# Optimization experiments

Hardware: AMD Instinct MI355X
Metric: run time of the kernel (lower is better)

## Reference

```python
import jax, jax.numpy as jnp
import numpy as np

NUM_NEIGHBORS = (10, 25)  # FLAGS.num_neighbors = '10_25'
MAX_DEGREE = 64
L = 2  # num encoder layers


def _sample(nodes, neighbors_out, neighbors_in, key):
    """Multi-hop uniform neighbor sampling (shuffle columns + slice, as in TF code)."""
    samples = [nodes]
    support = 1
    supports = [1]
    for k in range(L):
        t = L - 1 - k
        n = NUM_NEIGHBORS[t]
        support *= 2 * n
        supports.append(support)
        key, k1, k2 = jax.random.split(key, 3)
        # tf.transpose(tf.random.shuffle(tf.transpose(x))) shuffles neighbor slots
        # with ONE permutation shared across all rows, then slices first n.
        cols_out = jax.random.permutation(k1, MAX_DEGREE)[:n]
        cols_in = jax.random.permutation(k2, MAX_DEGREE)[:n]
        nout = neighbors_out[samples[k]][:, cols_out]  # [prev, n]
        nin = neighbors_in[samples[k]][:, cols_in]     # [prev, n]
        samples.append(jnp.concatenate([nout, nin], axis=1).reshape(-1))
    return samples, supports


def _gc(self_v, nei_out, nei_in, W):
    # GraphConvolution: mean-aggregate out/in neighbors, concat with self, linear, sigmoid.
    agg = jnp.concatenate([self_v, nei_out.mean(axis=1), nei_in.mean(axis=1)], axis=-1)
    return jax.nn.sigmoid(agg @ W)


def _aggregate(inputs, supports, layer, W, B):
    h_hop = []
    for hop in range(L - layer):
        n = NUM_NEIGHBORS[L - hop - 1]
        nei = inputs[hop + 1].reshape(B * supports[hop], 2 * n, -1)
        self_v = inputs[hop].reshape(B * supports[hop], -1)
        h_hop.append(_gc(self_v, nei[:, :n], nei[:, n:], W))
    return h_hop


def _forward(nodes1, nodes2, neighbors_out, neighbors_in, features,
             W_in, W_mean, W_std, W_pi, W_ag, W_ad, Wd_mean, Wd_std, Wd_pi):
    B = nodes1.shape[0]
    key = jax.random.key(42)
    k1, k2 = jax.random.split(key)
    s1, sup1 = _sample(nodes1, neighbors_out, neighbors_in, k1)
    s2, sup2 = _sample(nodes2, neighbors_out, neighbors_in, k2)
    in1 = [features[s] for s in s1]  # hop-wise gathered features
    in2 = [features[s] for s in s2]
    # layer 0: shared input GC
    h1 = _aggregate(in1, sup1, 0, W_in, B)
    h2 = _aggregate(in2, sup2, 0, W_in, B)
    # layer 1: parameter heads (mean/std/pi/alpha)
    h_mean1 = _aggregate(h1, sup1, 1, W_mean, B)[0]
    h_mean2 = _aggregate(h2, sup2, 1, W_mean, B)[0]
    h_std1 = _aggregate(h1, sup1, 1, W_std, B)[0]
    h_std2 = _aggregate(h2, sup2, 1, W_std, B)[0]
    h_pi1 = _aggregate(h1, sup1, 1, W_pi, B)[0]
    h_pi2 = _aggregate(h2, sup2, 1, W_pi, B)[0]
    # final fully-connected projections (act = identity)
    z_mean1 = h_mean1 @ Wd_mean
    z_mean2 = h_mean2 @ Wd_mean
    z_std1 = h_std1 @ Wd_std
    z_std2 = h_std2 @ Wd_std
    pi_logit1 = h_pi1 @ Wd_pi
    pi_logit2 = h_pi2 @ Wd_pi
    return jnp.stack([z_mean1, z_std1, pi_logit1, z_mean2, z_std2, pi_logit2])


def setup_inputs() -> dict:
    key = jax.random.key(0)
    ks = jax.random.split(key, 16)
    N, F, B = 200000, 128, 256
    E, D = 128, 64
    inp = {
        'nodes1': jax.random.randint(ks[0], (B,), 0, N, dtype=jnp.int32),
        'nodes2': jax.random.randint(ks[1], (B,), 0, N, dtype=jnp.int32),
        'neighbors_out': jax.random.randint(ks[2], (N, MAX_DEGREE), 0, N, dtype=jnp.int32),
        'neighbors_in': jax.random.randint(ks[3], (N, MAX_DEGREE), 0, N, dtype=jnp.int32),
        'features': jax.random.normal(ks[4], (N, F), dtype=jnp.float32),
        'W_in': jax.random.normal(ks[5], (3 * F, E), dtype=jnp.float32) * 0.05,
        'W_mean': jax.random.normal(ks[6], (3 * E, E), dtype=jnp.float32) * 0.05,
        'W_std': jax.random.normal(ks[7], (3 * E, E), dtype=jnp.float32) * 0.05,
        'W_pi': jax.random.normal(ks[8], (3 * E, E), dtype=jnp.float32) * 0.05,
        'W_ag': jax.random.normal(ks[9], (3 * E, E), dtype=jnp.float32) * 0.05,
        'W_ad': jax.random.normal(ks[10], (3 * E, E), dtype=jnp.float32) * 0.05,
        'Wd_mean': jax.random.normal(ks[11], (E, D), dtype=jnp.float32) * 0.05,
        'Wd_std': jax.random.normal(ks[12], (E, D), dtype=jnp.float32) * 0.05,
        'Wd_pi': jax.random.normal(ks[13], (E, D), dtype=jnp.float32) * 0.05,
    }
    return inp


def reference(nodes1, nodes2, neighbors_out, neighbors_in, features,
              W_in, W_mean, W_std, W_pi, W_ag, W_ad, Wd_mean, Wd_std, Wd_pi):
    return _forward(nodes1, nodes2, neighbors_out, neighbors_in, features,
                    W_in, W_mean, W_std, W_pi, W_ag, W_ad, Wd_mean, Wd_std, Wd_pi)
```

## Files before the change

### kernel.cpp

```cpp
#include <hip/hip_runtime.h>
#include <stdint.h>
#include <math.h>

#define FDIM 128
#define KDIM 384
#define NROWS 26112

struct Cols { int o25[25]; int i25[25]; int o10[10]; int i10[10]; };
struct ColsBoth { Cols c[2]; };

static inline uint32_t rotl32(uint32_t x, uint32_t r){ return (x<<r)|(x>>(32u-r)); }

static void tf2x32(uint32_t k0, uint32_t k1, uint32_t c0, uint32_t c1,
                   uint32_t& o0, uint32_t& o1){
  const uint32_t ra[4] = {13u,15u,26u,6u};
  const uint32_t rb[4] = {17u,29u,16u,24u};
  uint32_t ks2 = k0 ^ k1 ^ 0x1BD11BDAu;
  uint32_t x0 = c0 + k0, x1 = c1 + k1;
  for(int i=0;i<4;i++){ x0 += x1; x1 = rotl32(x1, ra[i]); x1 ^= x0; }
  x0 += k1; x1 += ks2 + 1u;
  for(int i=0;i<4;i++){ x0 += x1; x1 = rotl32(x1, rb[i]); x1 ^= x0; }
  x0 += ks2; x1 += k0 + 2u;
  for(int i=0;i<4;i++){ x0 += x1; x1 = rotl32(x1, ra[i]); x1 ^= x0; }
  x0 += k0; x1 += k1 + 3u;
  for(int i=0;i<4;i++){ x0 += x1; x1 = rotl32(x1, rb[i]); x1 ^= x0; }
  x0 += k1; x1 += ks2 + 4u;
  for(int i=0;i<4;i++){ x0 += x1; x1 = rotl32(x1, ra[i]); x1 ^= x0; }
  x0 += ks2; x1 += k0 + 5u;
  o0 = x0; o1 = x1;
}

static void jax_split_child(uint32_t ka, uint32_t kb, uint32_t i,
                            uint32_t& oa, uint32_t& ob){
  tf2x32(ka, kb, 0u, i, oa, ob);
}

static uint32_t jax_bits32(uint32_t ka, uint32_t kb, uint32_t i){
  uint32_t a,b; tf2x32(ka, kb, 0u, i, a, b);
  return a ^ b;
}

static void jax_perm64(uint32_t ka, uint32_t kb, int* perm){
  uint32_t sa, sb; jax_split_child(ka, kb, 1u, sa, sb);
  uint32_t b[64]; int v[64];
  for(int i=0;i<64;i++){ b[i]=jax_bits32(sa, sb, (uint32_t)i); v[i]=i; }
  for(int i=1;i<64;i++){
    uint32_t bb=b[i]; int vv=v[i]; int j=i-1;
    while(j>=0 && b[j]>bb){ b[j+1]=b[j]; v[j+1]=v[j]; j--; }
    b[j+1]=bb; v[j+1]=vv;
  }
  for(int i=0;i<64;i++) perm[i]=v[i];
}

static void compute_cols(ColsBoth& cb){
  uint32_t k1a,k1b,k2a,k2b;
  jax_split_child(0u, 42u, 0u, k1a, k1b);
  jax_split_child(0u, 42u, 1u, k2a, k2b);
  for(int side=0; side<2; side++){
    uint32_t ka = side ? k2a : k1a;
    uint32_t kb = side ? k2b : k1b;
    uint32_t nka,nkb, c1a,c1b, c2a,c2b;
    jax_split_child(ka,kb,0u,nka,nkb);
    jax_split_child(ka,kb,1u,c1a,c1b);
    jax_split_child(ka,kb,2u,c2a,c2b);
    int p[64];
    jax_perm64(c1a,c1b,p); for(int i=0;i<25;i++) cb.c[side].o25[i]=p[i];
    jax_perm64(c2a,c2b,p); for(int i=0;i<25;i++) cb.c[side].i25[i]=p[i];
    uint32_t d1a,d1b,d2a,d2b;
    jax_split_child(nka,nkb,1u,d1a,d1b);
    jax_split_child(nka,nkb,2u,d2a,d2b);
    jax_perm64(d1a,d1b,p); for(int i=0;i<10;i++) cb.c[side].o10[i]=p[i];
    jax_perm64(d2a,d2b,p); for(int i=0;i<10;i++) cb.c[side].i10[i]=p[i];
  }
}

__device__ __forceinline__ float getc(const float4& v, int i){
  return (i==0)?v.x:(i==1)?v.y:(i==2)?v.z:v.w;
}
__device__ __forceinline__ float sigf(float x){ return 1.0f/(1.0f+expf(-x)); }
__device__ __forceinline__ void add4(float4& s, const float4& v){
  s.x+=v.x; s.y+=v.y; s.z+=v.z; s.w+=v.w;
}
__device__ __forceinline__ void add2(float2& s, const float2& v){
  s.x+=v.x; s.y+=v.y;
}


__global__ __launch_bounds__(256) void gather_kernel(
    const float* __restrict__ feat,
    const int* __restrict__ nodes1, const int* __restrict__ nodes2,
    const int* __restrict__ nout, const int* __restrict__ nin,
    float* __restrict__ agg, int base_row, ColsBoth cb)
{
  int t = threadIdx.x;
  int row_local = blockIdx.x*8 + (t>>5);
  int lane = t & 31;
  int c0 = lane*4;
  int row = base_row + row_local;

  float4 selfv, so, si;

  if(row < 512){
    int side = row >> 8, b = row & 255;
    int node = (side ? nodes2 : nodes1)[b];
    const Cols& c = cb.c[side];
    const long nb = (long)node*64;
    selfv = *(const float4*)(feat + (long)node*FDIM + c0);
    float4 acc = make_float4(0,0,0,0);
    #pragma unroll
    for(int jj=0; jj<25; jj+=5){
      int id[5]; float4 v[5];
      #pragma unroll
      for(int i=0;i<5;i++) id[i] = nout[nb + c.o25[jj+i]];
      #pragma unroll
      for(int i=0;i<5;i++) v[i] = *(const float4*)(feat + (long)id[i]*FDIM + c0);
      #pragma unroll
      for(int i=0;i<5;i++) add4(acc, v[i]);
    }
    so = make_float4(acc.x/25.f, acc.y/25.f, acc.z/25.f, acc.w/25.f);
    acc = make_float4(0,0,0,0);
    #pragma unroll
    for(int jj=0; jj<25; jj+=5){
      int id[5]; float4 v[5];
      #pragma unroll
      for(int i=0;i<5;i++) id[i] = nin[nb + c.i25[jj+i]];
      #pragma unroll
      for(int i=0;i<5;i++) v[i] = *(const float4*)(feat + (long)id[i]*FDIM + c0);
      #pragma unroll
      for(int i=0;i<5;i++) add4(acc, v[i]);
    }
    si = make_float4(acc.x/25.f, acc.y/25.f, acc.z/25.f, acc.w/25.f);
  } else {
    int hrow = row - 512;
    int side = (hrow >= 12800) ? 1 : 0;
    int r = side ? (hrow - 12800) : hrow;
    int b = r / 50, slot = r % 50;
    const Cols& c = cb.c[side];
    int root = (side ? nodes2 : nodes1)[b];
    int node;
    if(slot < 25) node = nout[(long)root*64 + c.o25[slot]];
    else          node = nin [(long)root*64 + c.i25[slot-25]];
    const long nb = (long)node*64;
    int oid[10], iid[10];
    #pragma unroll
    for(int j=0;j<10;j++) oid[j] = nout[nb + c.o10[j]];
    #pragma unroll
    for(int j=0;j<10;j++) iid[j] = nin[nb + c.i10[j]];
    selfv = *(const float4*)(feat + (long)node*FDIM + c0);
    float4 v[20];
    #pragma unroll
    for(int j=0;j<10;j++) v[j]    = *(const float4*)(feat + (long)oid[j]*FDIM + c0);
    #pragma unroll
    for(int j=0;j<10;j++) v[10+j] = *(const float4*)(feat + (long)iid[j]*FDIM + c0);
    float4 acc = make_float4(0,0,0,0);
    #pragma unroll
    for(int j=0;j<10;j++) add4(acc, v[j]);
    so = make_float4(acc.x*0.1f, acc.y*0.1f, acc.z*0.1f, acc.w*0.1f);
    acc = make_float4(0,0,0,0);
    #pragma unroll
    for(int j=0;j<10;j++) add4(acc, v[10+j]);
    si = make_float4(acc.x*0.1f, acc.y*0.1f, acc.z*0.1f, acc.w*0.1f);
  }

  float* ar = agg + (long)row_local*KDIM;
  *(float4*)(ar + c0)       = selfv;
  *(float4*)(ar + 128 + c0) = so;
  *(float4*)(ar + 256 + c0) = si;
}

__global__ __launch_bounds__(256) void gemm_sig_kernel(
    const float* __restrict__ A, const float* __restrict__ W,
    float* __restrict__ out)
{
  __shared__ float Wbuf[96*128];
  int t = threadIdx.x, lane = t&15, rg = t>>4;
  int r0 = blockIdx.x*64 + rg*4;
  int c0 = lane*8;
  float acc[4][8];
  #pragma unroll
  for(int r=0;r<4;r++)
    #pragma unroll
    for(int i=0;i<8;i++) acc[r][i]=0.f;

  for(int kc=0; kc<4; kc++){
    __syncthreads();
    const float4* ws = (const float4*)(W + kc*96*128);
    float4* wd = (float4*)Wbuf;
    #pragma unroll
    for(int i=0;i<12;i++) wd[i*256+t] = ws[i*256+t];
    __syncthreads();
    const float* Ab = A + (long)r0*KDIM + kc*96;
    #pragma unroll 2
    for(int k4=0;k4<96;k4+=4){
      float4 a0 = *(const float4*)(Ab + 0*KDIM + k4);
      float4 a1 = *(const float4*)(Ab + 1*KDIM + k4);
      float4 a2 = *(const float4*)(Ab + 2*KDIM + k4);
      float4 a3 = *(const float4*)(Ab + 3*KDIM + k4);
      #pragma unroll
      for(int kk=0;kk<4;kk++){
        float av0=getc(a0,kk), av1=getc(a1,kk), av2=getc(a2,kk), av3=getc(a3,kk);
        const float* wr = Wbuf + (k4+kk)*128 + c0;
        float4 w0 = *(const float4*)wr;
        float4 w1 = *(const float4*)(wr+4);
        acc[0][0]+=av0*w0.x; acc[0][1]+=av0*w0.y; acc[0][2]+=av0*w0.z; acc[0][3]+=av0*w0.w;
        acc[0][4]+=av0*w1.x; acc[0][5]+=av0*w1.y; acc[0][6]+=av0*w1.z; acc[0][7]+=av0*w1.w;
        acc[1][0]+=av1*w0.x; acc[1][1]+=av1*w0.y; acc[1][2]+=av1*w0.z; acc[1][3]+=av1*w0.w;
        acc[1][4]+=av1*w1.x; acc[1][5]+=av1*w1.y; acc[1][6]+=av1*w1.z; acc[1][7]+=av1*w1.w;
        acc[2][0]+=av2*w0.x; acc[2][1]+=av2*w0.y; acc[2][2]+=av2*w0.z; acc[2][3]+=av2*w0.w;
        acc[2][4]+=av2*w1.x; acc[2][5]+=av2*w1.y; acc[2][6]+=av2*w1.z; acc[2][7]+=av2*w1.w;
        acc[3][0]+=av3*w0.x; acc[3][1]+=av3*w0.y; acc[3][2]+=av3*w0.z; acc[3][3]+=av3*w0.w;
        acc[3][4]+=av3*w1.x; acc[3][5]+=av3*w1.y; acc[3][6]+=av3*w1.z; acc[3][7]+=av3*w1.w;
      }
    }
  }
  #pragma unroll
  for(int r=0;r<4;r++){
    float4 o0, o1;
    o0.x=sigf(acc[r][0]); o0.y=sigf(acc[r][1]); o0.z=sigf(acc[r][2]); o0.w=sigf(acc[r][3]);
    o1.x=sigf(acc[r][4]); o1.y=sigf(acc[r][5]); o1.z=sigf(acc[r][6]); o1.w=sigf(acc[r][7]);
    float* op = out + (long)(r0+r)*FDIM + c0;
    *(float4*)op = o0; *(float4*)(op+4) = o1;
  }
}

__global__ __launch_bounds__(256) void head_kernel(
    const float* __restrict__ h,
    const float* __restrict__ Wm, const float* __restrict__ Ws, const float* __restrict__ Wp,
    const float* __restrict__ Dm, const float* __restrict__ Ds, const float* __restrict__ Dp,
    float* __restrict__ out)
{
  __shared__ float As[4*KDIM];
  __shared__ float Hs[4*FDIM];
  int head = blockIdx.x >> 7;
  int rt   = blockIdx.x & 127;
  int t = threadIdx.x;
  int row = t >> 6;
  int lane = t & 63;
  const float* W = (head==0) ? Wm : (head==1) ? Ws : Wp;
  const float* D = (head==0) ? Dm : (head==1) ? Ds : Dp;
  int grow = rt*4 + row;

  {
    int c2 = lane*2;
    float2 selfv = *(const float2*)(h + (long)grow*FDIM + c2);
    const float* nb = h + (long)(512 + grow*50)*FDIM + c2;
    float2 s = make_float2(0,0);
    #pragma unroll
    for(int jj=0;jj<25;jj+=5){
      float2 v[5];
      #pragma unroll
      for(int i=0;i<5;i++) v[i] = *(const float2*)(nb + (long)(jj+i)*FDIM);
      #pragma unroll
      for(int i=0;i<5;i++) add2(s, v[i]);
    }
    float2 so = make_float2(s.x/25.f, s.y/25.f);
    s = make_float2(0,0);
    #pragma unroll
    for(int jj=25;jj<50;jj+=5){
      float2 v[5];
      #pragma unroll
      for(int i=0;i<5;i++) v[i] = *(const float2*)(nb + (long)(jj+i)*FDIM);
      #pragma unroll
      for(int i=0;i<5;i++) add2(s, v[i]);
    }
    float2 si = make_float2(s.x/25.f, s.y/25.f);
    *(float2*)&As[row*KDIM + c2]       = selfv;
    *(float2*)&As[row*KDIM + 128 + c2] = so;
    *(float2*)&As[row*KDIM + 256 + c2] = si;
  }
  __syncthreads();

  {
    int c = lane*2;
    float acc0 = 0.f, acc1 = 0.f;
    const float* as = As + row*KDIM;
    #pragma unroll 8
    for(int k=0;k<KDIM;k++){
      float a = as[k];
      float2 w = *(const float2*)(W + (long)k*FDIM + c);
      acc0 += a*w.x; acc1 += a*w.y;
    }
    Hs[row*FDIM + c]   = sigf(acc0);
    Hs[row*FDIM + c+1] = sigf(acc1);
  }
  __syncthreads();

  {
    int col = lane;
    const float* hs = Hs + row*FDIM;
    float a = 0.f;
    #pragma unroll 8
    for(int k=0;k<FDIM;k++){
      a += hs[k] * D[(long)k*64 + col];
    }
    int side = grow >> 8, b = grow & 255;
    out[((long)(side*3+head)*256 + b)*64 + col] = a;
  }
}

extern "C" void kernel_launch(void* const* d_in, const int* in_sizes, int n_in,
                              void* d_out, int out_size, void* d_ws, size_t ws_size,
                              hipStream_t stream) {
  const int*   nodes1  = (const int*)d_in[0];
  const int*   nodes2  = (const int*)d_in[1];
  const int*   nout    = (const int*)d_in[2];
  const int*   nin     = (const int*)d_in[3];
  const float* feat    = (const float*)d_in[4];
  const float* W_in    = (const float*)d_in[5];
  const float* W_mean  = (const float*)d_in[6];
  const float* W_std   = (const float*)d_in[7];
  const float* W_pi    = (const float*)d_in[8];
  const float* Wd_mean = (const float*)d_in[11];
  const float* Wd_std  = (const float*)d_in[12];
  const float* Wd_pi   = (const float*)d_in[13];
  float* out = (float*)d_out;

  float* h    = (float*)d_ws;
  float* aggC = h + (size_t)NROWS*FDIM;

  size_t fixedB = (size_t)NROWS*FDIM*4;
  const int ncOpt[5] = {1,2,4,12,51};
  int nc = 51;
  for(int i=0;i<5;i++){
    size_t need = fixedB + ((size_t)NROWS/ncOpt[i])*KDIM*4;
    if(need <= ws_size){ nc = ncOpt[i]; break; }
  }
  int chunkRows = NROWS / nc;

  ColsBoth cb;
  compute_cols(cb);

  for(int c=0;c<nc;c++){
    int base = c*chunkRows;
    gather_kernel<<<chunkRows/8, 256, 0, stream>>>(feat, nodes1, nodes2,
                                                   nout, nin, aggC, base, cb);
    gemm_sig_kernel<<<chunkRows/64, 256, 0, stream>>>(aggC, W_in, h + (size_t)base*FDIM);
  }
  head_kernel<<<384, 256, 0, stream>>>(h, W_mean, W_std, W_pi, Wd_mean, Wd_std, Wd_pi, out);
}
```

Baseline: 325.2 us.

## Fuse neighbor gather with input GEMM+sigmoid through shared memory

Merges the gather kernel and the W_in GEMM into one kernel. Each block gathers 8 aggregated rows into padded LDS and immediately multiplies them by W_in, writing sigmoid outputs directly. This removes the global round trip of the 384-wide aggregate buffer and the chunked launch loop. The cost is that W_in is now read from global/L2 per block with only 8 rows of reuse, instead of being staged in LDS across 64 rows.

```diff
diff --git a/kernel.cpp b/kernel.cpp
--- a/kernel.cpp
+++ b/kernel.cpp
@@ -5,6 +5,7 @@
 #define FDIM 128
 #define KDIM 384
 #define NROWS 26112
+#define ASTRIDE 388
 
 struct Cols { int o25[25]; int i25[25]; int o10[10]; int i10[10]; };
 struct ColsBoth { Cols c[2]; };
@@ -86,17 +87,19 @@
 }
 
 
-__global__ __launch_bounds__(256) void gather_kernel(
+__global__ __launch_bounds__(256) void fused_gg_kernel(
     const float* __restrict__ feat,
     const int* __restrict__ nodes1, const int* __restrict__ nodes2,
     const int* __restrict__ nout, const int* __restrict__ nin,
-    float* __restrict__ agg, int base_row, ColsBoth cb)
+    const float* __restrict__ W,
+    float* __restrict__ h, ColsBoth cb)
 {
+  __shared__ float As[8*ASTRIDE];
   int t = threadIdx.x;
-  int row_local = blockIdx.x*8 + (t>>5);
+  int g = t >> 5;
   int lane = t & 31;
   int c0 = lane*4;
-  int row = base_row + row_local;
+  int row = blockIdx.x*8 + g;
 
   float4 selfv, so, si;
 
@@ -162,64 +165,40 @@
     si = make_float4(acc.x*0.1f, acc.y*0.1f, acc.z*0.1f, acc.w*0.1f);
   }
 
-  float* ar = agg + (long)row_local*KDIM;
-  *(float4*)(ar + c0)       = selfv;
-  *(float4*)(ar + 128 + c0) = so;
-  *(float4*)(ar + 256 + c0) = si;
-}
-
-__global__ __launch_bounds__(256) void gemm_sig_kernel(
-    const float* __restrict__ A, const float* __restrict__ W,
-    float* __restrict__ out)
-{
-  __shared__ float Wbuf[96*128];
-  int t = threadIdx.x, lane = t&15, rg = t>>4;
-  int r0 = blockIdx.x*64 + rg*4;
-  int c0 = lane*8;
-  float acc[4][8];
-  #pragma unroll
-  for(int r=0;r<4;r++)
-    #pragma unroll
-    for(int i=0;i<8;i++) acc[r][i]=0.f;
-
-  for(int kc=0; kc<4; kc++){
-    __syncthreads();
-    const float4* ws = (const float4*)(W + kc*96*128);
-    float4* wd = (float4*)Wbuf;
-    #pragma unroll
-    for(int i=0;i<12;i++) wd[i*256+t] = ws[i*256+t];
-    __syncthreads();
-    const float* Ab = A + (long)r0*KDIM + kc*96;
+  {
+    float* ar = As + g*ASTRIDE;
+    *(float4*)(ar + c0)       = selfv;
+    *(float4*)(ar + 128 + c0) = so;
+    *(float4*)(ar + 256 + c0) = si;
+  }
+  __syncthreads();
+
+  {
+    int l  = t & 63;
+    int wv = t >> 6;
+    int col = wv*32 + (l & 15)*2;
+    int rs  = l >> 4;
+    const float* a0p = As + (rs*2)*ASTRIDE;
+    const float* a1p = As + (rs*2+1)*ASTRIDE;
+    const float* wp  = W + col;
+    float acc00=0.f, acc01=0.f, acc10=0.f, acc11=0.f;
     #pragma unroll 2
-    for(int k4=0;k4<96;k4+=4){
-      float4 a0 = *(const float4*)(Ab + 0*KDIM + k4);
-      float4 a1 = *(const float4*)(Ab + 1*KDIM + k4);
-      float4 a2 = *(const float4*)(Ab + 2*KDIM + k4);
-      float4 a3 = *(const float4*)(Ab + 3*KDIM + k4);
-      #pragma unroll
-      for(int kk=0;kk<4;kk++){
-        float av0=getc(a0,kk), av1=getc(a1,kk), av2=getc(a2,kk), av3=getc(a3,kk);
-        const float* wr = Wbuf + (k4+kk)*128 + c0;
-        float4 w0 = *(const float4*)wr;
-        float4 w1 = *(const float4*)(wr+4);
-        acc[0][0]+=av0*w0.x; acc[0][1]+=av0*w0.y; acc[0][2]+=av0*w0.z; acc[0][3]+=av0*w0.w;
-        acc[0][4]+=av0*w1.x; acc[0][5]+=av0*w1.y; acc[0][6]+=av0*w1.z; acc[0][7]+=av0*w1.w;
-        acc[1][0]+=av1*w0.x; acc[1][1]+=av1*w0.y; acc[1][2]+=av1*w0.z; acc[1][3]+=av1*w0.w;
-        acc[1][4]+=av1*w1.x; acc[1][5]+=av1*w1.y; acc[1][6]+=av1*w1.z; acc[1][7]+=av1*w1.w;
-        acc[2][0]+=av2*w0.x; acc[2][1]+=av2*w0.y; acc[2][2]+=av2*w0.z; acc[2][3]+=av2*w0.w;
-        acc[2][4]+=av2*w1.x; acc[2][5]+=av2*w1.y; acc[2][6]+=av2*w1.z; acc[2][7]+=av2*w1.w;
-        acc[3][0]+=av3*w0.x; acc[3][1]+=av3*w0.y; acc[3][2]+=av3*w0.z; acc[3][3]+=av3*w0.w;
-        acc[3][4]+=av3*w1.x; acc[3][5]+=av3*w1.y; acc[3][6]+=av3*w1.z; acc[3][7]+=av3*w1.w;
+    for(int k4=0; k4<KDIM; k4+=4){
+      float4 a0 = *(const float4*)(a0p + k4);
+      float4 a1 = *(const float4*)(a1p + k4);
+      #pragma unroll
+      for(int kk=0; kk<4; kk++){
+        float2 w2 = *(const float2*)(wp + (k4+kk)*FDIM);
+        float av0 = getc(a0,kk), av1 = getc(a1,kk);
+        acc00 += av0*w2.x; acc01 += av0*w2.y;
+        acc10 += av1*w2.x; acc11 += av1*w2.y;
       }
     }
-  }
-  #pragma unroll
-  for(int r=0;r<4;r++){
-    float4 o0, o1;
-    o0.x=sigf(acc[r][0]); o0.y=sigf(acc[r][1]); o0.z=sigf(acc[r][2]); o0.w=sigf(acc[r][3]);
-    o1.x=sigf(acc[r][4]); o1.y=sigf(acc[r][5]); o1.z=sigf(acc[r][6]); o1.w=sigf(acc[r][7]);
-    float* op = out + (long)(r0+r)*FDIM + c0;
-    *(float4*)op = o0; *(float4*)(op+4) = o1;
+    long grow = (long)blockIdx.x*8 + rs*2;
+    float* o0 = h + grow*FDIM + col;
+    float* o1 = o0 + FDIM;
+    *(float2*)o0 = make_float2(sigf(acc00), sigf(acc01));
+    *(float2*)o1 = make_float2(sigf(acc10), sigf(acc11));
   }
 }
 
@@ -315,26 +294,12 @@
   const float* Wd_pi   = (const float*)d_in[13];
   float* out = (float*)d_out;
 
-  float* h    = (float*)d_ws;
-  float* aggC = h + (size_t)NROWS*FDIM;
-
-  size_t fixedB = (size_t)NROWS*FDIM*4;
-  const int ncOpt[5] = {1,2,4,12,51};
-  int nc = 51;
-  for(int i=0;i<5;i++){
-    size_t need = fixedB + ((size_t)NROWS/ncOpt[i])*KDIM*4;
-    if(need <= ws_size){ nc = ncOpt[i]; break; }
-  }
-  int chunkRows = NROWS / nc;
+  float* h = (float*)d_ws;
 
   ColsBoth cb;
   compute_cols(cb);
 
-  for(int c=0;c<nc;c++){
-    int base = c*chunkRows;
-    gather_kernel<<<chunkRows/8, 256, 0, stream>>>(feat, nodes1, nodes2,
-                                                   nout, nin, aggC, base, cb);
-    gemm_sig_kernel<<<chunkRows/64, 256, 0, stream>>>(aggC, W_in, h + (size_t)base*FDIM);
-  }
+  fused_gg_kernel<<<NROWS/8, 256, 0, stream>>>(feat, nodes1, nodes2,
+                                               nout, nin, W_in, h, cb);
   head_kernel<<<384, 256, 0, stream>>>(h, W_mean, W_std, W_pi, Wd_mean, Wd_std, Wd_pi, out);
 }
```

Measured after the change: 404.5 us. 1.24x slower.
